# Optimization experiments

Hardware: AMD Instinct MI355X
Metric: run time of the kernel (lower is better)

## Reference

```python
import jax, jax.numpy as jnp
import numpy as np
from jax import lax

EPS = 1e-5
DN = ('NCHW', 'OIHW', 'NCHW')
# torch F.pad order is (W_left, W_right, H_top, H_bottom); lax padding is ((H_lo,H_hi),(W_lo,W_hi))
PAD1 = ((1, 1), (1, 1))  # conv (3,3), pad (1,1,1,1)
PAD2 = ((1, 0), (1, 1))  # conv (2,3), pad (1,1,1,0)
PAD3 = ((1, 1), (1, 0))  # conv (3,2), pad (1,0,1,1)
PAD4 = ((1, 0), (1, 0))  # conv (2,2), pad (1,0,1,0)


def _conv(x, w, b, pad):
    y = lax.conv_general_dilated(x, w, (1, 1), pad, dimension_numbers=DN)
    return y + b[None, :, None, None]


def _bn(x, gamma, beta):
    # BatchNorm2d in training mode: biased batch stats over (N, H, W)
    m = jnp.mean(x, axis=(0, 2, 3), keepdims=True)
    v = jnp.var(x, axis=(0, 2, 3), keepdims=True)
    return (x - m) * lax.rsqrt(v + EPS) * gamma[None, :, None, None] + beta[None, :, None, None]


def _interleave(a, b, c, d):
    # a,b,c,d: [B,C,H,W] -> [B,C,2H,2W]; A->(even,even), B->(odd,even), C->(even,odd), D->(odd,odd)
    B, C, H, W = a.shape
    top = jnp.stack([a, c], axis=4).reshape(B, C, H, 2 * W)  # even rows
    bot = jnp.stack([b, d], axis=4).reshape(B, C, H, 2 * W)  # odd rows
    return jnp.stack([top, bot], axis=3).reshape(B, C, 2 * H, 2 * W)


def _unpool_as_conv(x, wA, bA, wB, bB, wC, bC, wD, bD, gamma, beta, relu):
    oA = _conv(x, wA, bA, PAD1)
    oB = _conv(x, wB, bB, PAD2)
    oC = _conv(x, wC, bC, PAD3)
    oD = _conv(x, wD, bD, PAD4)
    y = _interleave(oA, oB, oC, oD)
    y = _bn(y, gamma, beta)
    if relu:
        y = jax.nn.relu(y)
    return y


def _forward(x, w1, b1, w2, b2, w3, b3, w4, b4, w5, b5, w6, b6, w7, b7, w8, b8,
             w9, b9, g11, be11, g12, be12, g2, be2):
    out1 = _unpool_as_conv(x, w1, b1, w2, b2, w3, b3, w4, b4, g11, be11, relu=True)
    out1 = _conv(out1, w9, b9, ((1, 1), (1, 1)))
    out1 = _bn(out1, g2, be2)
    out2 = _unpool_as_conv(x, w5, b5, w6, b6, w7, b7, w8, b8, g12, be12, relu=False)
    return jax.nn.relu(out1 + out2)


def setup_inputs() -> dict:
    key = jax.random.key(0)
    B, Cin, Cout, H, W = 16, 512, 256, 32, 32
    ks = jax.random.split(key, 32)
    it = iter(ks)

    def w(shape, fan_in):
        return jax.random.normal(next(it), shape, dtype=jnp.float32) * (1.0 / np.sqrt(fan_in))

    inp = {"x": jax.random.normal(next(it), (B, Cin, H, W), dtype=jnp.float32)}
    # branch 1 convs
    inp["w1"], inp["b1"] = w((Cout, Cin, 3, 3), Cin * 9), w((Cout,), Cin * 9)
    inp["w2"], inp["b2"] = w((Cout, Cin, 2, 3), Cin * 6), w((Cout,), Cin * 6)
    inp["w3"], inp["b3"] = w((Cout, Cin, 3, 2), Cin * 6), w((Cout,), Cin * 6)
    inp["w4"], inp["b4"] = w((Cout, Cin, 2, 2), Cin * 4), w((Cout,), Cin * 4)
    # branch 2 convs
    inp["w5"], inp["b5"] = w((Cout, Cin, 3, 3), Cin * 9), w((Cout,), Cin * 9)
    inp["w6"], inp["b6"] = w((Cout, Cin, 2, 3), Cin * 6), w((Cout,), Cin * 6)
    inp["w7"], inp["b7"] = w((Cout, Cin, 3, 2), Cin * 6), w((Cout,), Cin * 6)
    inp["w8"], inp["b8"] = w((Cout, Cin, 2, 2), Cin * 4), w((Cout,), Cin * 4)
    # conv9
    inp["w9"], inp["b9"] = w((Cout, Cout, 3, 3), Cout * 9), w((Cout,), Cout * 9)
    # batchnorms
    inp["g11"], inp["be11"] = jnp.ones((Cout,), jnp.float32), jnp.zeros((Cout,), jnp.float32)
    inp["g12"], inp["be12"] = jnp.ones((Cout,), jnp.float32), jnp.zeros((Cout,), jnp.float32)
    inp["g2"], inp["be2"] = jnp.ones((Cout,), jnp.float32), jnp.zeros((Cout,), jnp.float32)
    return inp


def reference(x, w1, b1, w2, b2, w3, b3, w4, b4, w5, b5, w6, b6, w7, b7, w8, b8,
              w9, b9, g11, be11, g12, be12, g2, be2):
    return _forward(x, w1, b1, w2, b2, w3, b3, w4, b4, w5, b5, w6, b6, w7, b7, w8, b8,
                    w9, b9, g11, be11, g12, be12, g2, be2)
```

## Files before the change

### kernel.cpp

```cpp
#include <hip/hip_runtime.h>
#include <stdint.h>


typedef __bf16 bf16x8 __attribute__((ext_vector_type(8)));
typedef float floatx4 __attribute__((ext_vector_type(4)));

typedef __attribute__((address_space(3))) uint32_t lds32_t;
typedef __attribute__((address_space(1))) const uint32_t glb32_t;

__device__ __forceinline__ void load_lds16(const uint16_t* g, uint16_t* l) {
  __builtin_amdgcn_global_load_lds((glb32_t*)g, (lds32_t*)l, 16, 0, 0);
}

__device__ __forceinline__ float bf2f(uint32_t u) {
  union { uint32_t i; float f; } v;
  v.i = u << 16;
  return v.f;
}
__device__ __forceinline__ uint16_t f2bf(float f) {
  union { float f; uint32_t i; } v;
  v.f = f;
  uint32_t r = v.i + 0x7fff + ((v.i >> 16) & 1);
  return (uint16_t)(r >> 16);
}
__device__ __forceinline__ float load_in(const void* p, size_t i, bool isbf) {
  return isbf ? bf2f(((const uint16_t*)p)[i]) : ((const float*)p)[i];
}

__device__ __forceinline__ int cls_ntaps(int cls) { return cls == 0 ? 9 : (cls == 3 ? 4 : 6); }
__device__ __forceinline__ size_t cls_off(int cls) {
  return cls == 0 ? 0u : (cls == 1 ? 2359296u : (cls == 2 ? 3932160u : 5505024u));
}
__device__ __forceinline__ void cls_tap(int cls, int r, int& dy, int& dx) {
  if (cls >= 2) { dy = r >> 1; dx = r & 1; }
  else { dy = r / 3; dx = r - 3 * (r / 3); }
}

__global__ void detect_dtype(const uint32_t* __restrict__ xw, uint32_t* __restrict__ flag) {
  int t = threadIdx.x;
  int cnt = 0;
#pragma unroll
  for (int k = 0; k < 16; ++k) {
    uint32_t u = xw[t + k * 256];
    uint32_t e = (u >> 7) & 0xFF;
    cnt += (e >= 100 && e <= 140) ? 1 : 0;
  }
  __shared__ int rs[256];
  rs[t] = cnt;
  __syncthreads();
  for (int o = 128; o > 0; o >>= 1) {
    if (t < o) rs[t] += rs[t + o];
    __syncthreads();
  }
  if (t == 0) flag[0] = (rs[0] > 2048) ? 1u : 0u;
}

__global__ __launch_bounds__(256) void pack_w_unpool(
    const void* wa, const void* wb, const void* wc, const void* wd,
    const void* we, const void* wf, const void* wg, const void* wh,
    const uint32_t* __restrict__ flag, uint16_t* __restrict__ Wp) {
  const void* ws[8] = {wa, wb, wc, wd, we, wf, wg, wh};
  __shared__ uint16_t wl[12800];
  const bool isbf = flag[0] != 0;
  const int t = threadIdx.x;
  const int m = blockIdx.x;
  const int branch = m >> 8, cout = m & 255;
  int base = 0;
#pragma unroll
  for (int cls = 0; cls < 4; ++cls) {
    const int ntap = cls_ntaps(cls);
    const int cnt = 512 * ntap;
    const void* src = ws[branch * 4 + cls];
    const size_t s0 = (size_t)cout * cnt;
    for (int idx = t; idx < cnt; idx += 256)
      wl[base + idx] = f2bf(load_in(src, s0 + idx, isbf));
    base += cnt;
  }
  __syncthreads();
  for (int kc = t; kc < 12800; kc += 256) {
    int cls, kk, b2, ntap;
    if (kc < 4608) { cls = 0; kk = kc; b2 = 0; ntap = 9; }
    else if (kc < 7680) { cls = 1; kk = kc - 4608; b2 = 4608; ntap = 6; }
    else if (kc < 10752) { cls = 2; kk = kc - 7680; b2 = 7680; ntap = 6; }
    else { cls = 3; kk = kc - 10752; b2 = 10752; ntap = 4; }
    const int r = kk >> 9, cin = kk & 511;
    const int Kcls = ntap << 9;
    Wp[cls_off(cls) + (size_t)m * Kcls + kk] = wl[b2 + cin * ntap + r];
  }
}

__global__ void pack_w9b(const void* __restrict__ w9,
                         const void* b1, const void* b2, const void* b3, const void* b4,
                         const void* b5, const void* b6, const void* b7, const void* b8,
                         const void* b9, const uint32_t* __restrict__ flag,
                         uint16_t* __restrict__ Wp9, float* __restrict__ bpk,
                         float* __restrict__ b9pk) {
  const bool isbf = flag[0] != 0;
  int m = blockIdx.y;
  int k = blockIdx.x * 256 + threadIdx.x;
  int r = k >> 8, cin = k & 255;
  int dy = r / 3, dx = r - dy * 3;
  Wp9[(size_t)m * 2304 + k] = f2bf(load_in(w9, (size_t)((m * 256 + cin) * 3 + dy) * 3 + dx, isbf));
  if (blockIdx.x == 0 && m < 9) {
    const void* bs[8] = {b1, b2, b3, b4, b5, b6, b7, b8};
    int t = threadIdx.x;
    if (m < 8) {
      int cls = m >> 1, branch = m & 1;
      bpk[m * 256 + t] = load_in(bs[branch * 4 + cls], t, isbf);
    } else {
      b9pk[t] = load_in(b9, t, isbf);
    }
  }
}

__global__ __launch_bounds__(256) void pad_x_kernel(const void* __restrict__ x,
                                                    const uint32_t* __restrict__ flag,
                                                    uint16_t* __restrict__ xp) {
  __shared__ uint16_t lt[512 * 32];
  const bool isbf = flag[0] != 0;
  const int t = threadIdx.x;
  const int b = blockIdx.x >> 5, i = blockIdx.x & 31;
  const uint4 zero4 = make_uint4(0u, 0u, 0u, 0u);
  {
    const size_t row = (size_t)(b * 34 + i + 1) * 34;
    if (t < 64) *(uint4*)&xp[(row + 0) * 512 + t * 8] = zero4;
    else if (t < 128) *(uint4*)&xp[(row + 33) * 512 + (t - 64) * 8] = zero4;
  }
  if (i == 0) {
    const size_t r0 = (size_t)(b * 34 + 0) * 34 * 512;
    for (int idx = t; idx < 2176; idx += 256) *(uint4*)&xp[r0 + idx * 8] = zero4;
  }
  if (i == 31) {
    const size_t r33 = (size_t)(b * 34 + 33) * 34 * 512;
    for (int idx = t; idx < 2176; idx += 256) *(uint4*)&xp[r33 + idx * 8] = zero4;
  }
  const int jg = t & 7;
  for (int it = 0; it < 16; ++it) {
    const int c = (t >> 3) + it * 32;
    const size_t src = ((size_t)(b * 512 + c) * 32 + i) * 32 + jg * 4;
    uint16_t v[4];
    if (isbf) {
      uint2 d = *(const uint2*)((const uint16_t*)x + src);
      v[0] = (uint16_t)(d.x & 0xffff); v[1] = (uint16_t)(d.x >> 16);
      v[2] = (uint16_t)(d.y & 0xffff); v[3] = (uint16_t)(d.y >> 16);
    } else {
      float4 d = *(const float4*)((const float*)x + src);
      v[0] = f2bf(d.x); v[1] = f2bf(d.y); v[2] = f2bf(d.z); v[3] = f2bf(d.w);
    }
    const int sw = ((c >> 3) & 15) << 1;
#pragma unroll
    for (int e = 0; e < 4; ++e) lt[c * 32 + ((jg * 4 + e) ^ sw)] = v[e];
  }
  __syncthreads();
  const int cg = t & 63;
  for (int it = 0; it < 8; ++it) {
    const int j = it * 4 + (t >> 6);
    uint16_t v[8];
#pragma unroll
    for (int e = 0; e < 8; ++e) {
      const int R = cg * 8 + e;
      v[e] = lt[R * 32 + (j ^ ((cg & 15) << 1))];
    }
    *(uint4*)&xp[((size_t)(b * 34 + i + 1) * 34 + (j + 1)) * 512 + cg * 8] = *(const uint4*)v;
  }
}

template <int CIN, int IMGW_SHIFT, int PIXB_SHIFT, int PADW, int MODE>
__device__ __forceinline__ void gemm_conv_body(const uint16_t* __restrict__ Wp,
                                               const uint16_t* __restrict__ xp,
                                               const float* __restrict__ bias,
                                               uint16_t* __restrict__ o0,
                                               uint16_t* __restrict__ o1) {
  constexpr int IMGW = 1 << IMGW_SHIFT;
  constexpr int CSH = (CIN == 512) ? 9 : 8;
  __shared__ uint16_t As[2 * 128 * 32];
  __shared__ uint16_t Bs[2 * 128 * 32];

  const int tid = threadIdx.x;
  const int wave = tid >> 6, lane = tid & 63;

  int cls, mt, nt;
  if (MODE == 0) {
    const int bid = blockIdx.x;
    cls = bid >> 9;
    const int w = bid & 511;
    mt = w >> 7;
    nt = w & 127;
  } else {
    cls = 0;
    mt = blockIdx.x >> 9;
    nt = blockIdx.x & 511;
  }
  const int n0 = nt * 128;
  const int ntaps = (MODE == 0) ? cls_ntaps(cls) : 9;
  const int Krow = ntaps * CIN;
  const int NT = Krow >> 6;
  const int mrow0 = mt * 128;
  const uint16_t* Wbase = (MODE == 0) ? Wp + cls_off(cls) : Wp;

  const int srow = lane >> 2;
  const int scol = (((lane & 3) ^ ((lane >> 3) & 3)) << 3);

  const uint16_t* aS[2];
#pragma unroll
  for (int g = 0; g < 2; ++g)
    aS[g] = Wbase + (size_t)(mrow0 + wave * 32 + g * 16 + srow) * Krow + scol;

  auto pixb = [&](int n) -> size_t {
    const int bb = n >> PIXB_SHIFT;
    const int rem = n & ((1 << PIXB_SHIFT) - 1);
    const int hh = rem >> IMGW_SHIFT;
    const int ww = rem & (IMGW - 1);
    return ((size_t)(bb * PADW + hh) * PADW + ww) * CIN;
  };
  const uint16_t* bS[2];
#pragma unroll
  for (int g = 0; g < 2; ++g)
    bS[g] = xp + pixb(n0 + wave * 32 + g * 16 + srow) + scol;

  uint16_t* aD = &As[wave * 1024];
  uint16_t* bD = &Bs[wave * 1024];

  auto stageA = [&](int kh, int k0) {
#pragma unroll
    for (int g = 0; g < 2; ++g)
      load_lds16(aS[g] + k0 + kh * 32, aD + kh * 4096 + g * 512);
  };
  auto stageB = [&](int kh, size_t bo) {
#pragma unroll
    for (int g = 0; g < 2; ++g)
      load_lds16(bS[g] + bo + kh * 32, bD + kh * 4096 + g * 512);
  };
  auto bofff = [&](int t) -> size_t {
    const int k0 = t << 6;
    const int r = k0 >> CSH;
    int dy, dx;
    if (MODE == 0) cls_tap(cls, r, dy, dx);
    else { dy = r / 3; dx = r - 3 * dy; }
    return (size_t)(dy * PADW + dx) * CIN + (k0 & (CIN - 1));
  };

  floatx4 acc[4][4];
#pragma unroll
  for (int i = 0; i < 4; ++i)
#pragma unroll
    for (int j = 0; j < 4; ++j) acc[i][j] = floatx4{0.f, 0.f, 0.f, 0.f};

  const int wm = wave >> 1, wn = wave & 1;
  const int fl = lane & 15, kg = lane >> 4;
  const int eoff = ((kg ^ ((fl >> 1) & 3)) << 3);
  const int aoff = (wm * 64 + fl) * 32 + eoff;
  const int boff_r = (wn * 64 + fl) * 32 + eoff;

  for (int t = 0; t < NT; ++t) {
    const int k0 = t << 6;
    const size_t bo = bofff(t);
    stageA(0, k0); stageB(0, bo);
    stageA(1, k0); stageB(1, bo);
    __syncthreads();
#pragma unroll
    for (int kh = 0; kh < 2; ++kh) {
      bf16x8 af[4], bfr[4];
#pragma unroll
      for (int i = 0; i < 4; ++i) af[i] = *(const bf16x8*)&As[kh * 4096 + aoff + i * 512];
#pragma unroll
      for (int j = 0; j < 4; ++j) bfr[j] = *(const bf16x8*)&Bs[kh * 4096 + boff_r + j * 512];
      __builtin_amdgcn_s_setprio(1);
#pragma unroll
      for (int i = 0; i < 4; ++i)
#pragma unroll
        for (int j = 0; j < 4; ++j)
          acc[i][j] = __builtin_amdgcn_mfma_f32_16x16x32_bf16(af[i], bfr[j], acc[i][j], 0, 0, 0);
      __builtin_amdgcn_s_setprio(0);
    }
    __syncthreads();
  }

#pragma unroll
  for (int i = 0; i < 4; ++i) {
#pragma unroll
    for (int reg = 0; reg < 4; ++reg) {
      const int mloc = mrow0 + wm * 64 + i * 16 + kg * 4 + reg;
      if (MODE == 0) {
        const int branch = mloc >> 8, cout = mloc & 255;
        const float bv = bias[cls * 512 + mloc];
        uint16_t* o = branch ? o1 : o0;
#pragma unroll
        for (int j4 = 0; j4 < 4; ++j4) {
          const int n = n0 + wn * 64 + j4 * 16 + fl;
          const int bb = n >> 10, hh = (n >> 5) & 31, ww = n & 31;
          o[((size_t)((cls * 16 + bb) * 256 + cout) << 10) + (hh << 5) + ww] =
              f2bf(acc[i][j4][reg] + bv);
        }
      } else {
        const float bv = bias[mloc];
#pragma unroll
        for (int j4 = 0; j4 < 4; ++j4) {
          const int n = n0 + wn * 64 + j4 * 16 + fl;
          const int bb = n >> 12, hh = (n >> 6) & 63, ww = n & 63;
          o0[((size_t)((bb * 256 + mloc) * 64 + hh) << 6) + ww] = f2bf(acc[i][j4][reg] + bv);
        }
      }
    }
  }
}

__global__ __launch_bounds__(256, 4) void gemm_unpool(const uint16_t* __restrict__ Wp,
                                                      const uint16_t* __restrict__ xp,
                                                      const float* __restrict__ bias,
                                                      uint16_t* __restrict__ o0,
                                                      uint16_t* __restrict__ o1) {
  gemm_conv_body<512, 5, 10, 34, 0>(Wp, xp, bias, o0, o1);
}
__global__ __launch_bounds__(256, 4) void gemm_conv9(const uint16_t* __restrict__ Wp,
                                                     const uint16_t* __restrict__ xp,
                                                     const float* __restrict__ bias,
                                                     uint16_t* __restrict__ o0,
                                                     uint16_t* __restrict__ o1) {
  gemm_conv_body<256, 6, 12, 66, 1>(Wp, xp, bias, o0, o1);
}

__global__ void bn_stats2(const uint16_t* __restrict__ y1, const uint16_t* __restrict__ y2,
                          const void* __restrict__ g1, const void* __restrict__ be1,
                          const void* __restrict__ g2, const void* __restrict__ be2,
                          const uint32_t* __restrict__ flag,
                          float2* __restrict__ o1, float2* __restrict__ o2) {
  const bool isbf = flag[0] != 0;
  const int sel = blockIdx.x >> 8;
  const int c = blockIdx.x & 255, t = threadIdx.x;
  const uint32_t* yu = (const uint32_t*)(sel ? y2 : y1);
  float s = 0.f, s2 = 0.f;
  for (int r = 0; r < 64; ++r) {
    size_t base = (size_t)(r * 256 + c) * 512;
#pragma unroll
    for (int k = 0; k < 2; ++k) {
      uint32_t v = yu[base + t + k * 256];
      float lo = bf2f(v & 0xffff), hi = bf2f(v >> 16);
      s += lo + hi;
      s2 += lo * lo + hi * hi;
    }
  }
  __shared__ float rs[256], rs2[256];
  rs[t] = s; rs2[t] = s2;
  __syncthreads();
  for (int off = 128; off > 0; off >>= 1) {
    if (t < off) { rs[t] += rs[t + off]; rs2[t] += rs2[t + off]; }
    __syncthreads();
  }
  if (t == 0) {
    float mean = rs[0] * (1.f / 65536.f);
    float var = rs2[0] * (1.f / 65536.f) - mean * mean;
    const void* gm = sel ? g2 : g1;
    const void* bt = sel ? be2 : be1;
    float scale = load_in(gm, c, isbf) * rsqrtf(var + 1e-5f);
    float shift = load_in(bt, c, isbf) - mean * scale;
    (sel ? o2 : o1)[c] = make_float2(scale, shift);
  }
}

__global__ void bn_stats(const uint16_t* __restrict__ y, const void* __restrict__ gamma,
                         const void* __restrict__ beta, const uint32_t* __restrict__ flag,
                         float2* __restrict__ out, int R) {
  const bool isbf = flag[0] != 0;
  int c = blockIdx.x, t = threadIdx.x;
  const uint32_t* yu = (const uint32_t*)y;
  const int rows = 32768 / R, kw = R / 256;
  float s = 0.f, s2 = 0.f;
  for (int r = 0; r < rows; ++r) {
    size_t base = (size_t)(r * 256 + c) * R;
    for (int k = 0; k < kw; ++k) {
      uint32_t v = yu[base + t + k * 256];
      float lo = bf2f(v & 0xffff), hi = bf2f(v >> 16);
      s += lo + hi;
      s2 += lo * lo + hi * hi;
    }
  }
  __shared__ float rs[256], rs2[256];
  rs[t] = s; rs2[t] = s2;
  __syncthreads();
  for (int off = 128; off > 0; off >>= 1) {
    if (t < off) { rs[t] += rs[t + off]; rs2[t] += rs2[t + off]; }
    __syncthreads();
  }
  if (t == 0) {
    float mean = rs[0] * (1.f / 65536.f);
    float var = rs2[0] * (1.f / 65536.f) - mean * mean;
    float scale = load_in(gamma, c, isbf) * rsqrtf(var + 1e-5f);
    float shift = load_in(beta, c, isbf) - mean * scale;
    out[c] = make_float2(scale, shift);
  }
}

__global__ __launch_bounds__(256) void u_fill(const uint16_t* __restrict__ y1,
                                              const float2* __restrict__ st,
                                              uint16_t* __restrict__ u) {
  __shared__ uint16_t lt[512 * 32];
  const int t = threadIdx.x;
  const int b = blockIdx.x >> 6, h = blockIdx.x & 63;
  const uint4 zero4 = make_uint4(0u, 0u, 0u, 0u);
  {
    const size_t row = (size_t)(b * 66 + h + 1) * 66;
    if (t < 32) *(uint4*)&u[(row + 0) * 256 + t * 8] = zero4;
    else if (t < 64) *(uint4*)&u[(row + 65) * 256 + (t - 32) * 8] = zero4;
  }
  if (h == 0) {
    const size_t r0 = (size_t)(b * 66 + 0) * 66 * 256;
    for (int idx = t; idx < 2112; idx += 256) *(uint4*)&u[r0 + idx * 8] = zero4;
  }
  if (h == 63) {
    const size_t r65 = (size_t)(b * 66 + 65) * 66 * 256;
    for (int idx = t; idx < 2112; idx += 256) *(uint4*)&u[r65 + idx * 8] = zero4;
  }
  const int clsE = h & 1, h2 = h >> 1;
  const int wg = t & 7;
  for (int it = 0; it < 16; ++it) {
    const int R = (t >> 3) + it * 32;
    const int p = R >> 8, c = R & 255;
    const int cls = clsE + 2 * p;
    const float2 ab = st[c];
    const size_t src = ((size_t)((cls * 16 + b) * 256 + c) << 10) + (h2 << 5) + wg * 4;
    uint2 d = *(const uint2*)&y1[src];
    uint16_t v[4];
    v[0] = f2bf(fmaxf(ab.x * bf2f(d.x & 0xffff) + ab.y, 0.f));
    v[1] = f2bf(fmaxf(ab.x * bf2f(d.x >> 16) + ab.y, 0.f));
    v[2] = f2bf(fmaxf(ab.x * bf2f(d.y & 0xffff) + ab.y, 0.f));
    v[3] = f2bf(fmaxf(ab.x * bf2f(d.y >> 16) + ab.y, 0.f));
    const int sw = ((R >> 3) & 15) << 1;
#pragma unroll
    for (int e = 0; e < 4; ++e) lt[R * 32 + ((wg * 4 + e) ^ sw)] = v[e];
  }
  __syncthreads();
  const int cg = t & 31;
  for (int it = 0; it < 8; ++it) {
    const int w = it * 8 + (t >> 5);
    const int p = w & 1, w2 = w >> 1;
    uint16_t v[8];
#pragma unroll
    for (int e = 0; e < 8; ++e) {
      const int R = p * 256 + cg * 8 + e;
      v[e] = lt[R * 32 + (w2 ^ (((R >> 3) & 15) << 1))];
    }
    *(uint4*)&u[((size_t)(b * 66 + h + 1) * 66 + (w + 1)) * 256 + cg * 8] = *(const uint4*)v;
  }
}

__global__ void final_kernel(const uint16_t* __restrict__ z, const uint16_t* __restrict__ y2,
                             const float2* __restrict__ st2, const float2* __restrict__ st12,
                             const uint32_t* __restrict__ flag, void* __restrict__ out) {
  const bool isbf = flag[0] != 0;
  size_t idx = ((size_t)blockIdx.x * 256 + threadIdx.x) * 8;
  const int b = (int)(idx >> 20), c = (int)((idx >> 12) & 255);
  const int H = (int)((idx >> 6) & 63), W0 = (int)(idx & 63);
  float2 a2 = st2[c], a12 = st12[c];
  const int clsE = H & 1;
  const size_t pE = (((size_t)((clsE * 16 + b) * 256 + c)) << 10) + ((H >> 1) << 5) + (W0 >> 1);
  const size_t pO = pE + ((size_t)2 << 22);
  uint2 e2 = *(const uint2*)&y2[pE];
  uint2 o2 = *(const uint2*)&y2[pO];
  uint16_t ye[4] = {(uint16_t)(e2.x & 0xffff), (uint16_t)(e2.x >> 16),
                    (uint16_t)(e2.y & 0xffff), (uint16_t)(e2.y >> 16)};
  uint16_t yo[4] = {(uint16_t)(o2.x & 0xffff), (uint16_t)(o2.x >> 16),
                    (uint16_t)(o2.y & 0xffff), (uint16_t)(o2.y >> 16)};
  uint4 vz = *(const uint4*)(z + idx);
  uint16_t zz[8] = {(uint16_t)(vz.x & 0xffff), (uint16_t)(vz.x >> 16),
                    (uint16_t)(vz.y & 0xffff), (uint16_t)(vz.y >> 16),
                    (uint16_t)(vz.z & 0xffff), (uint16_t)(vz.z >> 16),
                    (uint16_t)(vz.w & 0xffff), (uint16_t)(vz.w >> 16)};
  float r[8];
#pragma unroll
  for (int j = 0; j < 8; ++j) {
    uint16_t yv = (j & 1) ? yo[j >> 1] : ye[j >> 1];
    r[j] = fmaxf(a2.x * bf2f(zz[j]) + a2.y + a12.x * bf2f(yv) + a12.y, 0.f);
  }
  if (isbf) {
    uint4 vo;
    vo.x = (uint32_t)f2bf(r[0]) | ((uint32_t)f2bf(r[1]) << 16);
    vo.y = (uint32_t)f2bf(r[2]) | ((uint32_t)f2bf(r[3]) << 16);
    vo.z = (uint32_t)f2bf(r[4]) | ((uint32_t)f2bf(r[5]) << 16);
    vo.w = (uint32_t)f2bf(r[6]) | ((uint32_t)f2bf(r[7]) << 16);
    *(uint4*)((uint16_t*)out + idx) = vo;
  } else {
    float4* of = (float4*)((float*)out + idx);
    of[0] = make_float4(r[0], r[1], r[2], r[3]);
    of[1] = make_float4(r[4], r[5], r[6], r[7]);
  }
}

extern "C" void kernel_launch(void* const* d_in, const int* in_sizes, int n_in,
                              void* d_out, int out_size, void* d_ws, size_t ws_size,
                              hipStream_t stream) {
  const void* x = d_in[0];
  const void *w1 = d_in[1], *b1 = d_in[2], *w2 = d_in[3], *b2 = d_in[4];
  const void *w3 = d_in[5], *b3 = d_in[6], *w4 = d_in[7], *b4 = d_in[8];
  const void *w5 = d_in[9], *b5 = d_in[10], *w6 = d_in[11], *b6 = d_in[12];
  const void *w7 = d_in[13], *b7 = d_in[14], *w8 = d_in[15], *b8 = d_in[16];
  const void *w9 = d_in[17], *b9 = d_in[18];
  const void *g11 = d_in[19], *be11 = d_in[20], *g12 = d_in[21], *be12 = d_in[22];
  const void *g2 = d_in[23], *be2 = d_in[24];

  char* ws = (char*)d_ws;
  size_t off = 0;
  auto alloc = [&](size_t bytes) -> char* {
    char* p = ws + off;
    off = (off + bytes + 255) & ~(size_t)255;
    return p;
  };
  const size_t xp_bytes = (size_t)16 * 34 * 34 * 512 * 2;
  const size_t y_bytes = (size_t)16 * 256 * 64 * 64 * 2;
  const size_t u_bytes = (size_t)16 * 66 * 66 * 256 * 2;
  const size_t Wp_bytes = (size_t)512 * 12800 * 2;

  uint32_t* flag = (uint32_t*)alloc(256);
  uint16_t* Wp9 = (uint16_t*)alloc((size_t)256 * 2304 * 2);
  float* bpk = (float*)alloc(2048 * 4);
  float* b9pk = (float*)alloc(256 * 4);
  float2* st1a = (float2*)alloc(256 * 8);
  float2* st1b = (float2*)alloc(256 * 8);
  float2* st2 = (float2*)alloc(256 * 8);
  uint16_t* y1 = (uint16_t*)alloc(y_bytes);
  uint16_t* y2 = (uint16_t*)alloc(y_bytes);
  size_t wpal = (Wp_bytes + 255) & ~(size_t)255;
  size_t region_bytes = wpal + xp_bytes;
  if (region_bytes < u_bytes) region_bytes = u_bytes;
  char* region = alloc(region_bytes);
  uint16_t* Wp = (uint16_t*)region;
  uint16_t* xp = (uint16_t*)(region + wpal);
  uint16_t* u = (uint16_t*)region;
  uint16_t* z = y1;

  detect_dtype<<<1, 256, 0, stream>>>((const uint32_t*)x, flag);

  pack_w_unpool<<<512, 256, 0, stream>>>(w1, w2, w3, w4, w5, w6, w7, w8, flag, Wp);
  pack_w9b<<<dim3(9, 256), 256, 0, stream>>>(w9, b1, b2, b3, b4, b5, b6, b7, b8, b9,
                                             flag, Wp9, bpk, b9pk);
  pad_x_kernel<<<512, 256, 0, stream>>>(x, flag, xp);

  gemm_unpool<<<2048, 256, 0, stream>>>(Wp, xp, bpk, y1, y2);

  bn_stats2<<<512, 256, 0, stream>>>(y1, y2, g11, be11, g12, be12, flag, st1a, st1b);

  u_fill<<<1024, 256, 0, stream>>>(y1, st1a, u);

  gemm_conv9<<<1024, 256, 0, stream>>>(Wp9, u, b9pk, z, nullptr);

  bn_stats<<<256, 256, 0, stream>>>(z, g2, be2, flag, st2, 2048);

  final_kernel<<<8192, 256, 0, stream>>>(z, y2, st2, st1b, flag, d_out);
}
```

Measured before the change: 573.4 us.

## Fuse BatchNorm partial statistics into GEMM epilogues, replace stats passes with finalizers

Each GEMM epilogue now accumulates per-channel sum and sum-of-squares of the rounded bf16 outputs. It reduces them with wave shuffles and LDS, then writes per-tile partials to a buffer. Small finalize kernels sum the partials into scale and shift, replacing the two bn_stats kernels that re-read the full 32 MB outputs. This saves a memory-bound read pass per BN at the cost of extra epilogue work and a block-wide sync. The finalizers are tiny serial launches (1-2 blocks) that each loop over many partials.

```diff
diff --git a/kernel.cpp b/kernel.cpp
--- a/kernel.cpp
+++ b/kernel.cpp
@@ -170,7 +170,8 @@
                                                const uint16_t* __restrict__ xp,
                                                const float* __restrict__ bias,
                                                uint16_t* __restrict__ o0,
-                                               uint16_t* __restrict__ o1) {
+                                               uint16_t* __restrict__ o1,
+                                               float* __restrict__ P) {
   constexpr int IMGW = 1 << IMGW_SHIFT;
   constexpr int CSH = (CIN == 512) ? 9 : 8;
   __shared__ uint16_t As[2 * 128 * 32];
@@ -276,11 +277,13 @@
     __syncthreads();
   }
 
+  float* Lf = (float*)As;
 #pragma unroll
   for (int i = 0; i < 4; ++i) {
 #pragma unroll
     for (int reg = 0; reg < 4; ++reg) {
       const int mloc = mrow0 + wm * 64 + i * 16 + kg * 4 + reg;
+      float s = 0.f, s2 = 0.f;
       if (MODE == 0) {
         const int branch = mloc >> 8, cout = mloc & 255;
         const float bv = bias[cls * 512 + mloc];
@@ -288,20 +291,45 @@
 #pragma unroll
         for (int j4 = 0; j4 < 4; ++j4) {
           const int n = n0 + wn * 64 + j4 * 16 + fl;
+          const uint16_t hb = f2bf(acc[i][j4][reg] + bv);
+          const float v = bf2f(hb);
+          s += v; s2 += v * v;
           const int bb = n >> 10, hh = (n >> 5) & 31, ww = n & 31;
-          o[((size_t)((cls * 16 + bb) * 256 + cout) << 10) + (hh << 5) + ww] =
-              f2bf(acc[i][j4][reg] + bv);
+          o[((size_t)((cls * 16 + bb) * 256 + cout) << 10) + (hh << 5) + ww] = hb;
         }
       } else {
         const float bv = bias[mloc];
 #pragma unroll
         for (int j4 = 0; j4 < 4; ++j4) {
           const int n = n0 + wn * 64 + j4 * 16 + fl;
+          const uint16_t hb = f2bf(acc[i][j4][reg] + bv);
+          const float v = bf2f(hb);
+          s += v; s2 += v * v;
           const int bb = n >> 12, hh = (n >> 6) & 63, ww = n & 63;
-          o0[((size_t)((bb * 256 + mloc) * 64 + hh) << 6) + ww] = f2bf(acc[i][j4][reg] + bv);
+          o0[((size_t)((bb * 256 + mloc) * 64 + hh) << 6) + ww] = hb;
         }
       }
-    }
+#pragma unroll
+      for (int off = 1; off < 16; off <<= 1) {
+        s += __shfl_xor(s, off);
+        s2 += __shfl_xor(s2, off);
+      }
+      if (fl == 0) {
+        const int q = wm * 64 + i * 16 + kg * 4 + reg;
+        Lf[(q * 2 + wn) * 2 + 0] = s;
+        Lf[(q * 2 + wn) * 2 + 1] = s2;
+      }
+    }
+  }
+  __syncthreads();
+  if (tid < 128) {
+    const float s = Lf[(tid * 2 + 0) * 2 + 0] + Lf[(tid * 2 + 1) * 2 + 0];
+    const float s2 = Lf[(tid * 2 + 0) * 2 + 1] + Lf[(tid * 2 + 1) * 2 + 1];
+    size_t pi;
+    if (MODE == 0) pi = (((size_t)(cls * 4 + mt) * 128 + nt) * 128 + tid) * 2;
+    else pi = (((size_t)mt * 512 + nt) * 128 + tid) * 2;
+    P[pi] = s;
+    P[pi + 1] = s2;
   }
 }
 
@@ -309,86 +337,57 @@
                                                       const uint16_t* __restrict__ xp,
                                                       const float* __restrict__ bias,
                                                       uint16_t* __restrict__ o0,
-                                                      uint16_t* __restrict__ o1) {
-  gemm_conv_body<512, 5, 10, 34, 0>(Wp, xp, bias, o0, o1);
+                                                      uint16_t* __restrict__ o1,
+                                                      float* __restrict__ P) {
+  gemm_conv_body<512, 5, 10, 34, 0>(Wp, xp, bias, o0, o1, P);
 }
 __global__ __launch_bounds__(256, 4) void gemm_conv9(const uint16_t* __restrict__ Wp,
                                                      const uint16_t* __restrict__ xp,
                                                      const float* __restrict__ bias,
                                                      uint16_t* __restrict__ o0,
-                                                     uint16_t* __restrict__ o1) {
-  gemm_conv_body<256, 6, 12, 66, 1>(Wp, xp, bias, o0, o1);
-}
-
-__global__ void bn_stats2(const uint16_t* __restrict__ y1, const uint16_t* __restrict__ y2,
-                          const void* __restrict__ g1, const void* __restrict__ be1,
-                          const void* __restrict__ g2, const void* __restrict__ be2,
-                          const uint32_t* __restrict__ flag,
-                          float2* __restrict__ o1, float2* __restrict__ o2) {
+                                                     uint16_t* __restrict__ o1,
+                                                     float* __restrict__ P) {
+  gemm_conv_body<256, 6, 12, 66, 1>(Wp, xp, bias, o0, o1, P);
+}
+
+__global__ void bn_fin_unpool(const float* __restrict__ P,
+                              const void* __restrict__ g1, const void* __restrict__ be1,
+                              const void* __restrict__ g2, const void* __restrict__ be2,
+                              const uint32_t* __restrict__ flag,
+                              float2* __restrict__ o1, float2* __restrict__ o2) {
   const bool isbf = flag[0] != 0;
-  const int sel = blockIdx.x >> 8;
-  const int c = blockIdx.x & 255, t = threadIdx.x;
-  const uint32_t* yu = (const uint32_t*)(sel ? y2 : y1);
+  const int branch = blockIdx.x, c = threadIdx.x;
+  const int mloc = branch * 256 + c, mt = mloc >> 7, q = mloc & 127;
   float s = 0.f, s2 = 0.f;
-  for (int r = 0; r < 64; ++r) {
-    size_t base = (size_t)(r * 256 + c) * 512;
-#pragma unroll
-    for (int k = 0; k < 2; ++k) {
-      uint32_t v = yu[base + t + k * 256];
-      float lo = bf2f(v & 0xffff), hi = bf2f(v >> 16);
-      s += lo + hi;
-      s2 += lo * lo + hi * hi;
-    }
-  }
-  __shared__ float rs[256], rs2[256];
-  rs[t] = s; rs2[t] = s2;
-  __syncthreads();
-  for (int off = 128; off > 0; off >>= 1) {
-    if (t < off) { rs[t] += rs[t + off]; rs2[t] += rs2[t + off]; }
-    __syncthreads();
-  }
-  if (t == 0) {
-    float mean = rs[0] * (1.f / 65536.f);
-    float var = rs2[0] * (1.f / 65536.f) - mean * mean;
-    const void* gm = sel ? g2 : g1;
-    const void* bt = sel ? be2 : be1;
-    float scale = load_in(gm, c, isbf) * rsqrtf(var + 1e-5f);
-    float shift = load_in(bt, c, isbf) - mean * scale;
-    (sel ? o2 : o1)[c] = make_float2(scale, shift);
-  }
-}
-
-__global__ void bn_stats(const uint16_t* __restrict__ y, const void* __restrict__ gamma,
-                         const void* __restrict__ beta, const uint32_t* __restrict__ flag,
-                         float2* __restrict__ out, int R) {
+  for (int cls = 0; cls < 4; ++cls)
+    for (int nt = 0; nt < 128; ++nt) {
+      const float2 p = *(const float2*)&P[(((size_t)(cls * 4 + mt) * 128 + nt) * 128 + q) * 2];
+      s += p.x; s2 += p.y;
+    }
+  const float mean = s * (1.f / 65536.f);
+  const float var = s2 * (1.f / 65536.f) - mean * mean;
+  const void* gm = branch ? g2 : g1;
+  const void* bt = branch ? be2 : be1;
+  const float scale = load_in(gm, c, isbf) * rsqrtf(var + 1e-5f);
+  const float shift = load_in(bt, c, isbf) - mean * scale;
+  (branch ? o2 : o1)[c] = make_float2(scale, shift);
+}
+
+__global__ void bn_fin_conv9(const float* __restrict__ P,
+                             const void* __restrict__ gamma, const void* __restrict__ beta,
+                             const uint32_t* __restrict__ flag, float2* __restrict__ out) {
   const bool isbf = flag[0] != 0;
-  int c = blockIdx.x, t = threadIdx.x;
-  const uint32_t* yu = (const uint32_t*)y;
-  const int rows = 32768 / R, kw = R / 256;
+  const int c = threadIdx.x, mt = c >> 7, q = c & 127;
   float s = 0.f, s2 = 0.f;
-  for (int r = 0; r < rows; ++r) {
-    size_t base = (size_t)(r * 256 + c) * R;
-    for (int k = 0; k < kw; ++k) {
-      uint32_t v = yu[base + t + k * 256];
-      float lo = bf2f(v & 0xffff), hi = bf2f(v >> 16);
-      s += lo + hi;
-      s2 += lo * lo + hi * hi;
-    }
-  }
-  __shared__ float rs[256], rs2[256];
-  rs[t] = s; rs2[t] = s2;
-  __syncthreads();
-  for (int off = 128; off > 0; off >>= 1) {
-    if (t < off) { rs[t] += rs[t + off]; rs2[t] += rs2[t + off]; }
-    __syncthreads();
-  }
-  if (t == 0) {
-    float mean = rs[0] * (1.f / 65536.f);
-    float var = rs2[0] * (1.f / 65536.f) - mean * mean;
-    float scale = load_in(gamma, c, isbf) * rsqrtf(var + 1e-5f);
-    float shift = load_in(beta, c, isbf) - mean * scale;
-    out[c] = make_float2(scale, shift);
-  }
+  for (int nt = 0; nt < 512; ++nt) {
+    const float2 p = *(const float2*)&P[(((size_t)mt * 512 + nt) * 128 + q) * 2];
+    s += p.x; s2 += p.y;
+  }
+  const float mean = s * (1.f / 65536.f);
+  const float var = s2 * (1.f / 65536.f) - mean * mean;
+  const float scale = load_in(gamma, c, isbf) * rsqrtf(var + 1e-5f);
+  const float shift = load_in(beta, c, isbf) - mean * scale;
+  out[c] = make_float2(scale, shift);
 }
 
 __global__ __launch_bounds__(256) void u_fill(const uint16_t* __restrict__ y1,
@@ -517,6 +516,8 @@
   float2* st1a = (float2*)alloc(256 * 8);
   float2* st1b = (float2*)alloc(256 * 8);
   float2* st2 = (float2*)alloc(256 * 8);
+  float* P1 = (float*)alloc((size_t)4 * 4 * 128 * 128 * 2 * 4);
+  float* P9 = P1;
   uint16_t* y1 = (uint16_t*)alloc(y_bytes);
   uint16_t* y2 = (uint16_t*)alloc(y_bytes);
   size_t wpal = (Wp_bytes + 255) & ~(size_t)255;
@@ -535,15 +536,15 @@
                                              flag, Wp9, bpk, b9pk);
   pad_x_kernel<<<512, 256, 0, stream>>>(x, flag, xp);
 
-  gemm_unpool<<<2048, 256, 0, stream>>>(Wp, xp, bpk, y1, y2);
-
-  bn_stats2<<<512, 256, 0, stream>>>(y1, y2, g11, be11, g12, be12, flag, st1a, st1b);
+  gemm_unpool<<<2048, 256, 0, stream>>>(Wp, xp, bpk, y1, y2, P1);
+
+  bn_fin_unpool<<<2, 256, 0, stream>>>(P1, g11, be11, g12, be12, flag, st1a, st1b);
 
   u_fill<<<1024, 256, 0, stream>>>(y1, st1a, u);
 
-  gemm_conv9<<<1024, 256, 0, stream>>>(Wp9, u, b9pk, z, nullptr);
-
-  bn_stats<<<256, 256, 0, stream>>>(z, g2, be2, flag, st2, 2048);
+  gemm_conv9<<<1024, 256, 0, stream>>>(Wp9, u, b9pk, z, nullptr, P9);
+
+  bn_fin_conv9<<<1, 256, 0, stream>>>(P9, g2, be2, flag, st2);
 
   final_kernel<<<8192, 256, 0, stream>>>(z, y2, st2, st1b, flag, d_out);
 }
```

Measured after the change: 581.9 us. Within noise of the previous version (+1.5%).
